# Performance work log

Measured on AMD Instinct MI355X. Metric: run time of the kernel, lower is better.

Reference implementation:

```python
import jax, jax.numpy as jnp
import numpy as np

B, TM, SM, V = 16, 128, 64, 1024
NEG = jnp.float32(-1e30)  # safe stand-in for -inf (avoids nan in grads)


def setup_inputs() -> dict:
    key = jax.random.key(0)
    k1, k2 = jax.random.split(key)
    acts = jax.random.normal(k1, (B * TM * (SM + 1), V), dtype=jnp.float32)
    labels = jax.random.randint(k2, (B, SM), 1, V, dtype=jnp.int32)
    input_lengths = jnp.full((B,), TM, dtype=jnp.int32)
    label_lengths = jnp.full((B,), SM, dtype=jnp.int32)
    return {"acts": acts, "labels": labels, "input_lengths": input_lengths,
            "label_lengths": label_lengths, "T_max": TM, "S_max": SM}


def _monotonic_rnnt_loss(acts, labels, input_lengths, label_lengths, T_max, S_max, blank=0):
    """Monotonic RNN-T: each time frame emits exactly one symbol (blank keeps
    label position, a label advances it). Loss = -log p(labels | acts).
    acts is packed row-major: row(b,t,s) = off_b + t*(S_b+1) + s."""
    Bq = labels.shape[0]
    N = acts.shape[0]
    T = input_lengths.astype(jnp.int32)
    S = label_lengths.astype(jnp.int32)
    Sp1 = S + 1
    sizes = T * Sp1
    off = jnp.concatenate([jnp.zeros((1,), jnp.int32), jnp.cumsum(sizes)[:-1]])

    # log-softmax normalizer per packed row (softmax done internally by the loss)
    lse = jax.scipy.special.logsumexp(acts, axis=1)  # [N]

    t_idx = jnp.arange(T_max)[None, :, None]          # [1,T,1]
    s_idx = jnp.arange(S_max + 1)[None, None, :]      # [1,1,S+1]
    rows = off[:, None, None] + t_idx * Sp1[:, None, None] + s_idx  # [B,T,S+1]
    rows_c = jnp.clip(rows, 0, N - 1)

    valid_b = (t_idx < T[:, None, None]) & (s_idx <= S[:, None, None])
    blank_lp = jnp.where(valid_b, acts[rows_c, blank] - lse[rows_c], NEG)  # [B,T,S+1]

    lab_rows = rows_c[:, :, :S_max]                   # [B,T,S]
    valid_l = (t_idx < T[:, None, None]) & (s_idx[:, :, :S_max] < S[:, None, None])
    # gather log p(y_{s+1} | b, t, s) without materializing [B,T,S,V]
    label_lp = jnp.where(valid_l,
                         acts[lab_rows, labels[:, None, :]] - lse[lab_rows], NEG)  # [B,T,S]

    blank_t = jnp.transpose(blank_lp, (1, 0, 2))  # [T,B,S+1]
    label_t = jnp.transpose(label_lp, (1, 0, 2))  # [T,B,S]

    alpha0 = jnp.full((Bq, S_max + 1), NEG, dtype=acts.dtype).at[:, 0].set(0.0)

    def step(alpha, inp):
        t, blp, llp = inp
        # stay (blank) or advance one label
        shifted = jnp.concatenate(
            [jnp.full((Bq, 1), NEG, dtype=acts.dtype), alpha[:, :-1] + llp], axis=1)
        new = jnp.logaddexp(alpha + blp, shifted)
        # freeze alpha past each sequence's last frame
        return jnp.where(t < T[:, None], new, alpha), None

    alpha, _ = jax.lax.scan(step, alpha0, (jnp.arange(T_max), blank_t, label_t))
    return -alpha[jnp.arange(Bq), S]


def reference(acts, labels, input_lengths, label_lengths, T_max, S_max):
    return _monotonic_rnnt_loss(acts, labels, input_lengths, label_lengths, T_max, S_max, blank=0)
```

## Files before the change

kernel.cpp:

```cpp
#include <hip/hip_runtime.h>
#include <math.h>

#define Bc 16
#define TM 128
#define SMAX 64
#define VV 1024
#define NEGF (-1e30f)
#define CELLS (Bc * TM * (SMAX + 1))

typedef float f32x4 __attribute__((ext_vector_type(4)));

__device__ __forceinline__ float wave_sum64(float v) {
  #pragma unroll
  for (int o = 32; o > 0; o >>= 1) v += __shfl_down(v, o);
  return __shfl(v, 0);
}
__device__ __forceinline__ float logaddexp_f(float a, float b) {
  float m = fmaxf(a, b);
  float d = fminf(a, b) - m;
  return m + __logf(1.0f + __expf(d));
}

#define RPW 16
#define NPAIR (RPW / 2)

__global__ __launch_bounds__(256, 4) void rnnt_lp_kernel(
    const float* __restrict__ acts, const int* __restrict__ labels,
    const int* __restrict__ Tlen, const int* __restrict__ Slen,
    float* __restrict__ blank_lp, float* __restrict__ label_lp)
{
  const int lane = threadIdx.x & 63;
  const int wv   = threadIdx.x >> 6;
  const int wave = blockIdx.x * 4 + wv;
  const int cbase = wave * RPW;
  if (cbase >= CELLS) return;

  const int bidx = lane & 15;
  const int Tb_l = Tlen[bidx];
  const int Sb_l = Slen[bidx];
  const int sz   = Tb_l * (Sb_l + 1);
  int incl = sz;
  #pragma unroll
  for (int o = 1; o < 16; o <<= 1) {
    int u = __shfl_up(incl, o);
    if (bidx >= o) incl += u;
  }
  const int excl = incl - sz;

  struct Geo {
    int lab_idx;
    int s, Sb, lab;
    long long row;
    bool val;
  };

  auto geo = [&](int cell) {
    Geo g;
    const int b   = cell / (TM * (SMAX + 1));
    const int rem = cell - b * (TM * (SMAX + 1));
    const int t   = rem / (SMAX + 1);
    g.s = rem - t * (SMAX + 1);
    const int Tb = __shfl(Tb_l, b);
    g.Sb = __shfl(Sb_l, b);
    const int off = __shfl(excl, b);
    g.row = (long long)off + (long long)t * (g.Sb + 1) + g.s;
    g.val = (t < Tb) && (g.s <= g.Sb);
    g.lab_idx = (b * TM + t) * SMAX + g.s;
    g.lab = (g.val && g.s < g.Sb) ? labels[b * SMAX + g.s] : -1;
    return g;
  };

  auto issue = [&](const Geo& g, f32x4* x) {
    if (g.val) {
      const f32x4* rp = (const f32x4*)(acts + g.row * (long long)VV) + lane;
      x[0] = rp[0];
      x[1] = rp[64];
      x[2] = rp[128];
      x[3] = rp[192];
    }
  };

  auto compute = [&](int cell, const Geo& g, const f32x4* x) {
    if (!g.val) {
      if (lane == 0) {
        blank_lp[cell] = NEGF;
        if (g.s < SMAX) label_lp[g.lab_idx] = NEGF;
      }
      return;
    }
    float p = 0.0f;
    #pragma unroll
    for (int q = 0; q < 4; ++q)
      p += __expf(x[q].x) + __expf(x[q].y) + __expf(x[q].z) + __expf(x[q].w);
    const float lse = __logf(wave_sum64(p));
    if (g.s < g.Sb) {
      const int f    = g.lab >> 2;
      const int comp = g.lab & 3;
      const int src  = f & 63;
      const int j    = f >> 6;
      f32x4 xx = (j == 0) ? x[0] : (j == 1) ? x[1] : (j == 2) ? x[2] : x[3];
      float v = (comp == 0) ? xx.x : (comp == 1) ? xx.y : (comp == 2) ? xx.z : xx.w;
      v = __shfl(v, src);
      if (lane == 0) label_lp[g.lab_idx] = v - lse;
    } else if (g.s < SMAX) {
      if (lane == 0) label_lp[g.lab_idx] = NEGF;
    }
    if (lane == 0) blank_lp[cell] = x[0].x - lse;
  };

  f32x4 xb[2][2][4];
  Geo   gb[2][2];

  gb[0][0] = geo(cbase + 0);
  gb[0][1] = geo(cbase + 1);
  issue(gb[0][0], xb[0][0]);
  issue(gb[0][1], xb[0][1]);

  #pragma unroll
  for (int i = 0; i < NPAIR; ++i) {
    const int cur = i & 1, nxt = cur ^ 1;
    if (i + 1 < NPAIR) {
      gb[nxt][0] = geo(cbase + 2 * i + 2);
      gb[nxt][1] = geo(cbase + 2 * i + 3);
      issue(gb[nxt][0], xb[nxt][0]);
      issue(gb[nxt][1], xb[nxt][1]);
    }
    compute(cbase + 2 * i + 0, gb[cur][0], xb[cur][0]);
    compute(cbase + 2 * i + 1, gb[cur][1], xb[cur][1]);
  }
}

__global__ __launch_bounds__(256) void rnnt_alpha_kernel(
    const float* __restrict__ blank_lp, const float* __restrict__ label_lp,
    const int* __restrict__ Tlen, const int* __restrict__ Slen,
    float* __restrict__ out)
{
  __shared__ __align__(16) float sb[TM * (SMAX + 1)];
  __shared__ __align__(16) float sl[TM * SMAX];
  const int b = blockIdx.x;
  const int tid = threadIdx.x;

  const float* gb = blank_lp + (size_t)b * TM * (SMAX + 1);
  const float* gl = label_lp + (size_t)b * TM * SMAX;
  for (int i = tid * 4; i < TM * (SMAX + 1); i += 256 * 4)
    *(float4*)&sb[i] = *(const float4*)&gb[i];
  for (int i = tid * 4; i < TM * SMAX; i += 256 * 4)
    *(float4*)&sl[i] = *(const float4*)&gl[i];
  __syncthreads();
  if (tid >= 64) return;

  const int lane = tid;
  const int Tb = Tlen[b], Sb = Slen[b];
  float a    = (lane == 0) ? 0.0f : NEGF;
  float a_hi = NEGF;

  for (int t = 0; t < Tb; ++t) {
    const float blp      = sb[t * (SMAX + 1) + lane];
    const float llp_prev = (lane >= 1) ? sl[t * SMAX + lane - 1] : NEGF;
    const float blp64    = sb[t * (SMAX + 1) + 64];
    const float llp63    = sl[t * SMAX + 63];
    const float a_prev   = __shfl_up(a, 1);
    const float a63      = __shfl(a, 63);
    const float newv = logaddexp_f(a + blp,
                                   (lane >= 1) ? (a_prev + llp_prev) : NEGF);
    const float new_hi = logaddexp_f(a_hi + blp64, a63 + llp63);
    a = newv;
    a_hi = new_hi;
  }

  const float via_shfl = __shfl(a, Sb & 63);
  const float aS = (Sb < 64) ? via_shfl : a_hi;
  if (lane == 0) out[b] = -aS;
}

extern "C" void kernel_launch(void* const* d_in, const int* in_sizes, int n_in,
                              void* d_out, int out_size, void* d_ws, size_t ws_size,
                              hipStream_t stream) {
  const float* acts  = (const float*)d_in[0];
  const int* labels  = (const int*)d_in[1];
  const int* Tlen    = (const int*)d_in[2];
  const int* Slen    = (const int*)d_in[3];
  float* out = (float*)d_out;

  float* blank_lp = (float*)d_ws;
  float* label_lp = blank_lp + Bc * TM * (SMAX + 1);

  const int waves_total  = (CELLS + RPW - 1) / RPW;
  const int blocks       = (waves_total + 3) / 4;
  rnnt_lp_kernel<<<blocks, 256, 0, stream>>>(
      acts, labels, Tlen, Slen, blank_lp, label_lp);
  rnnt_alpha_kernel<<<Bc, 256, 0, stream>>>(
      blank_lp, label_lp, Tlen, Slen, out);
}
```

Before: 726.0 us.

## Batch four rows per wave with all loads issued up front and interleaved reductions

Each wave now handles four rows instead of sixteen. It issues all four rows' 16B loads at once rather than running a two-deep software pipeline over sixteen rows, and it interleaves the four wave-wide butterfly reductions using xor shuffles. Row addresses are computed as 32-bit byte offsets instead of 64-bit, and the occupancy hint in launch bounds is dropped. The aim is more memory-level parallelism per wave and more waves in flight across the grid, at the cost of more registers held per row and four times as many workgroups.

```diff
diff --git a/kernel.cpp b/kernel.cpp
--- a/kernel.cpp
+++ b/kernel.cpp
@@ -10,30 +10,24 @@
 
 typedef float f32x4 __attribute__((ext_vector_type(4)));
 
-__device__ __forceinline__ float wave_sum64(float v) {
-  #pragma unroll
-  for (int o = 32; o > 0; o >>= 1) v += __shfl_down(v, o);
-  return __shfl(v, 0);
-}
 __device__ __forceinline__ float logaddexp_f(float a, float b) {
   float m = fmaxf(a, b);
   float d = fminf(a, b) - m;
   return m + __logf(1.0f + __expf(d));
 }
 
-#define RPW 16
-#define NPAIR (RPW / 2)
+#define RPG 4
 
-__global__ __launch_bounds__(256, 4) void rnnt_lp_kernel(
+__global__ __launch_bounds__(256) void rnnt_lp_kernel(
     const float* __restrict__ acts, const int* __restrict__ labels,
     const int* __restrict__ Tlen, const int* __restrict__ Slen,
     float* __restrict__ blank_lp, float* __restrict__ label_lp)
 {
   const int lane = threadIdx.x & 63;
   const int wv   = threadIdx.x >> 6;
-  const int wave = blockIdx.x * 4 + wv;
-  const int cbase = wave * RPW;
-  if (cbase >= CELLS) return;
+  const int grp  = blockIdx.x * 4 + wv;
+  const int cell0 = grp * RPG;
+  if (cell0 >= CELLS) return;
 
   const int bidx = lane & 15;
   const int Tb_l = Tlen[bidx];
@@ -47,86 +41,81 @@
   }
   const int excl = incl - sz;
 
-  struct Geo {
-    int lab_idx;
-    int s, Sb, lab;
-    long long row;
-    bool val;
-  };
+  int s_[RPG], Sb_[RPG], lab_[RPG], labidx_[RPG];
+  bool val_[RPG];
+  unsigned off_[RPG];
+  f32x4 x[RPG][4];
 
-  auto geo = [&](int cell) {
-    Geo g;
+  #pragma unroll
+  for (int k = 0; k < RPG; ++k) {
+    const int cell = cell0 + k;
     const int b   = cell / (TM * (SMAX + 1));
     const int rem = cell - b * (TM * (SMAX + 1));
     const int t   = rem / (SMAX + 1);
-    g.s = rem - t * (SMAX + 1);
-    const int Tb = __shfl(Tb_l, b);
-    g.Sb = __shfl(Sb_l, b);
-    const int off = __shfl(excl, b);
-    g.row = (long long)off + (long long)t * (g.Sb + 1) + g.s;
-    g.val = (t < Tb) && (g.s <= g.Sb);
-    g.lab_idx = (b * TM + t) * SMAX + g.s;
-    g.lab = (g.val && g.s < g.Sb) ? labels[b * SMAX + g.s] : -1;
-    return g;
-  };
+    const int s   = rem - t * (SMAX + 1);
+    const int Tb  = __shfl(Tb_l, b);
+    const int Sb  = __shfl(Sb_l, b);
+    const int rb  = __shfl(excl, b);
+    s_[k] = s; Sb_[k] = Sb;
+    labidx_[k] = (b * TM + t) * SMAX + s;
+    val_[k] = (t < Tb) && (s <= Sb);
+    const unsigned row = (unsigned)rb + (unsigned)t * (unsigned)(Sb + 1) + (unsigned)s;
+    off_[k] = row * (unsigned)(VV * 4);
+    lab_[k] = (val_[k] && s < Sb) ? labels[b * SMAX + s] : -1;
+  }
 
-  auto issue = [&](const Geo& g, f32x4* x) {
-    if (g.val) {
-      const f32x4* rp = (const f32x4*)(acts + g.row * (long long)VV) + lane;
-      x[0] = rp[0];
-      x[1] = rp[64];
-      x[2] = rp[128];
-      x[3] = rp[192];
+  #pragma unroll
+  for (int k = 0; k < RPG; ++k) {
+    if (val_[k]) {
+      const f32x4* rp = (const f32x4*)((const char*)acts + off_[k]) + lane;
+      x[k][0] = rp[0];
+      x[k][1] = rp[64];
+      x[k][2] = rp[128];
+      x[k][3] = rp[192];
     }
-  };
+  }
 
-  auto compute = [&](int cell, const Geo& g, const f32x4* x) {
-    if (!g.val) {
+  float p[RPG];
+  #pragma unroll
+  for (int k = 0; k < RPG; ++k) {
+    float q = 0.0f;
+    #pragma unroll
+    for (int j = 0; j < 4; ++j)
+      q += __expf(x[k][j].x) + __expf(x[k][j].y) +
+           __expf(x[k][j].z) + __expf(x[k][j].w);
+    p[k] = q;
+  }
+
+  #pragma unroll
+  for (int o = 1; o < 64; o <<= 1) {
+    #pragma unroll
+    for (int k = 0; k < RPG; ++k) p[k] += __shfl_xor(p[k], o);
+  }
+
+  #pragma unroll
+  for (int k = 0; k < RPG; ++k) {
+    const int cell = cell0 + k;
+    if (!val_[k]) {
       if (lane == 0) {
         blank_lp[cell] = NEGF;
-        if (g.s < SMAX) label_lp[g.lab_idx] = NEGF;
+        if (s_[k] < SMAX) label_lp[labidx_[k]] = NEGF;
       }
-      return;
+      continue;
     }
-    float p = 0.0f;
-    #pragma unroll
-    for (int q = 0; q < 4; ++q)
-      p += __expf(x[q].x) + __expf(x[q].y) + __expf(x[q].z) + __expf(x[q].w);
-    const float lse = __logf(wave_sum64(p));
-    if (g.s < g.Sb) {
-      const int f    = g.lab >> 2;
-      const int comp = g.lab & 3;
+    const float lse = __logf(p[k]);
+    if (s_[k] < Sb_[k]) {
+      const int f    = lab_[k] >> 2;
+      const int comp = lab_[k] & 3;
       const int src  = f & 63;
       const int j    = f >> 6;
-      f32x4 xx = (j == 0) ? x[0] : (j == 1) ? x[1] : (j == 2) ? x[2] : x[3];
+      f32x4 xx = (j == 0) ? x[k][0] : (j == 1) ? x[k][1] : (j == 2) ? x[k][2] : x[k][3];
       float v = (comp == 0) ? xx.x : (comp == 1) ? xx.y : (comp == 2) ? xx.z : xx.w;
       v = __shfl(v, src);
-      if (lane == 0) label_lp[g.lab_idx] = v - lse;
-    } else if (g.s < SMAX) {
-      if (lane == 0) label_lp[g.lab_idx] = NEGF;
+      if (lane == 0) label_lp[labidx_[k]] = v - lse;
+    } else if (s_[k] < SMAX) {
+      if (lane == 0) label_lp[labidx_[k]] = NEGF;
     }
-    if (lane == 0) blank_lp[cell] = x[0].x - lse;
-  };
-
-  f32x4 xb[2][2][4];
-  Geo   gb[2][2];
-
-  gb[0][0] = geo(cbase + 0);
-  gb[0][1] = geo(cbase + 1);
-  issue(gb[0][0], xb[0][0]);
-  issue(gb[0][1], xb[0][1]);
-
-  #pragma unroll
-  for (int i = 0; i < NPAIR; ++i) {
-    const int cur = i & 1, nxt = cur ^ 1;
-    if (i + 1 < NPAIR) {
-      gb[nxt][0] = geo(cbase + 2 * i + 2);
-      gb[nxt][1] = geo(cbase + 2 * i + 3);
-      issue(gb[nxt][0], xb[nxt][0]);
-      issue(gb[nxt][1], xb[nxt][1]);
-    }
-    compute(cbase + 2 * i + 0, gb[cur][0], xb[cur][0]);
-    compute(cbase + 2 * i + 1, gb[cur][1], xb[cur][1]);
+    if (lane == 0) blank_lp[cell] = x[k][0].x - lse;
   }
 }
 
@@ -185,8 +174,8 @@
   float* blank_lp = (float*)d_ws;
   float* label_lp = blank_lp + Bc * TM * (SMAX + 1);
 
-  const int waves_total  = (CELLS + RPW - 1) / RPW;
-  const int blocks       = (waves_total + 3) / 4;
+  const int groups = (CELLS + RPG - 1) / RPG;
+  const int blocks = (groups + 3) / 4;
   rnnt_lp_kernel<<<blocks, 256, 0, stream>>>(
       acts, labels, Tlen, Slen, blank_lp, label_lp);
   rnnt_alpha_kernel<<<Bc, 256, 0, stream>>>(
```

After: 716.2 us. No clear change (-1.4%).
